# Optimization experiments

Hardware: AMD Instinct MI355X
Metric: run time of the kernel (lower is better)

The kernel has to match this reference:

```python
import jax, jax.numpy as jnp
import numpy as np

GAMMA = 0.999      # EMA momentum
M_PROTO = 10       # prototypes per class
K_CLS = 201        # 200 classes + background
EPS_SK = 0.05      # sinkhorn temperature
SK_ITERS = 3       # sinkhorn iterations
THR = 0.5          # pseudo-gt threshold
D_BB = 768         # backbone dim
D = 512            # projected dim


def _ln(x, g, b, eps=1e-5):
    mu = x.mean(-1, keepdims=True)
    var = ((x - mu) ** 2).mean(-1, keepdims=True)
    return (x - mu) / jnp.sqrt(var + eps) * g + b


def _l2n(x, eps=1e-12):
    n = jnp.linalg.norm(x, axis=-1, keepdims=True)
    return x / jnp.maximum(n, eps)


def _pca_dir(A, niter=10):
    # rank-1 PCA direction (deterministic power iteration; mirrors torch.pca_lowrank(q=1, center=True))
    Ac = A - A.mean(0, keepdims=True)
    v = jnp.ones((A.shape[1],), A.dtype) / jnp.sqrt(jnp.asarray(A.shape[1], A.dtype))
    for _ in range(niter):
        v = Ac.T @ (Ac @ v)
        v = v / jnp.linalg.norm(v)
    u = Ac @ v
    return u / jnp.linalg.norm(u)


def setup_inputs() -> dict:
    key = jax.random.key(0)
    ks = jax.random.split(key, 6)
    B, HW = 16, 1024
    return dict(
        patch_tokens=jax.random.normal(ks[0], (B, HW, D_BB), jnp.float32),
        gt=jax.random.randint(ks[1], (B,), 0, K_CLS - 1),
        proj_w=jax.random.normal(ks[2], (D, D_BB), jnp.float32) * 0.02,
        proj_b=jnp.zeros((D,), jnp.float32),
        feat_g=jnp.ones((D,), jnp.float32),
        feat_b=jnp.zeros((D,), jnp.float32),
        mask_g=jnp.ones((K_CLS,), jnp.float32),
        mask_b=jnp.zeros((K_CLS,), jnp.float32),
        prototypes=jax.random.normal(ks[3], (K_CLS, M_PROTO, D), jnp.float32) * 0.02,
    )


def reference(patch_tokens, gt, proj_w, proj_b, feat_g, feat_b, mask_g, mask_b, prototypes):
    B, HW, _ = patch_tokens.shape
    H = W = int(np.sqrt(HW))
    N = B * HW

    # ----- ged_pseudo_gt (on detached tokens) -----
    U = _pca_dir(patch_tokens.reshape(-1, D_BB))            # [N]
    Us = (U - U.min()) / (U.max() - U.min())
    Us = Us.reshape(B, H, W)
    pseudo_gt = jnp.where(Us < THR, gt[:, None, None], K_CLS - 1)  # [B,H,W]

    # ----- projection + normalization -----
    f = patch_tokens @ proj_w.T + proj_b                    # [B,HW,D]
    _c = _l2n(_ln(f.reshape(N, D), feat_g, feat_b))         # [N,D]
    protos = _l2n(prototypes)                               # buffer is l2-normalized in-place
    masks = jnp.einsum('nd,kmd->nmk', _c, protos)           # [N,M,K] cosine sims
    out_flat = _ln(masks.max(axis=1), mask_g, mask_b)       # [N,K]
    out_seg = out_flat.reshape(B, H, W, K_CLS).transpose(0, 3, 1, 2)  # [B,K,H,W]

    # ----- prototype_learning (vectorized 201-class loop) -----
    gt_seg = pseudo_gt.reshape(-1)                          # [N] int
    pred = jnp.argmax(out_flat, axis=-1)
    correct = (gt_seg == pred).astype(_c.dtype)             # [N]
    proto_logits = _c @ protos.reshape(-1, D).T             # [N, K*M]

    sel = jax.nn.one_hot(gt_seg, K_CLS, dtype=_c.dtype)     # [N,K] class membership
    Bk = sel.sum(0)                                         # pixels per class
    Bk_safe = jnp.where(Bk > 0, Bk, 1.0)

    # masked per-class sinkhorn (all classes in parallel)
    Q = jnp.exp(masks / EPS_SK) * sel[:, None, :]           # [N,M,K]
    sQ = Q.sum((0, 1))                                      # [K]
    Q = Q / jnp.where(sQ > 0, sQ, 1.0)
    for _ in range(SK_ITERS):
        row = Q.sum(0, keepdims=True)                       # [1,M,K] sum over pixels
        Q = Q / jnp.where(row > 0, row, 1.0) / M_PROTO
        col = Q.sum(1, keepdims=True)                       # [N,1,K] sum over prototypes
        Q = Q / jnp.where(col > 0, col, 1.0) / Bk_safe
    Q = Q * Bk                                              # [N,M,K]

    Qn = jnp.take_along_axis(Q, gt_seg[:, None, None], axis=2)[:, :, 0]  # [N,M]
    idx = jnp.argmax(Qn, axis=1)                            # hard assignment per pixel
    proto_target = (idx + M_PROTO * gt_seg).astype(jnp.float32)

    # EMA update: q masked by prediction correctness (m_k applies to both m_q and c_q; m_k^2 = m_k)
    q = jax.nn.one_hot(idx, M_PROTO, dtype=_c.dtype) * correct[:, None]  # [N,M]
    fproto = jnp.einsum('nk,nm,nd->kmd', sel, q, _c)        # per-(class,proto) feature sums
    ncnt = jnp.einsum('nk,nm->km', sel, q)                  # assignment counts
    fnorm = _l2n(fproto)
    upd = (ncnt != 0)[:, :, None]
    new_protos = _l2n(jnp.where(upd, GAMMA * protos + (1.0 - GAMMA) * fnorm, protos))

    return out_seg, proto_logits, proto_target, pseudo_gt, new_protos
```

## Files before the change

### kernel.cpp

```cpp
#include <hip/hip_runtime.h>
#include <cstdint>
#include <cstddef>

typedef _Float16 half8  __attribute__((ext_vector_type(8)));
typedef _Float16 half4v __attribute__((ext_vector_type(4)));
typedef float    f32x4  __attribute__((ext_vector_type(4)));

static constexpr int HWPX = 1024;
static constexpr int NPX  = 16384;
static constexpr int DBB  = 768;
static constexpr int DD   = 512;
static constexpr int KC   = 201;
static constexpr int KM   = 2010;
static constexpr int KMP  = 2048;

static constexpr size_t OFF_XCH    = 0;
static constexpr size_t OFF_TP     = 491520;
static constexpr size_t OFF_COLP   = 492160;
static constexpr size_t OFF_ROW16  = 541312;
static constexpr size_t OFF_ROW3   = 670336;
static constexpr size_t OFF_ROW5   = 678400;
static constexpr size_t OFF_BK     = 686464;
static constexpr size_t OFF_NCNT   = 687488;
static constexpr size_t OFF_FPROTO = 695552;
static constexpr size_t OFF_MAXB   = 4812032;
static constexpr size_t ZTOTAL     = 17984768;
static constexpr size_t OFF_GTSEG  = 17984768;
static constexpr size_t OFF_CORR   = 18050304;
static constexpr size_t OFF_U      = 18115840;
static constexpr size_t OFF_PN     = 18246912;
static constexpr size_t OFF_P16    = 22363392;
static constexpr size_t OFF_C16    = 24460544;
static constexpr size_t OFF_QD     = 41237760;
static constexpr size_t OFF_W16    = 41893120;
static constexpr size_t OFF_MSF    = 42679552;

static constexpr size_t OUT_SEG = 0;
static constexpr size_t OUT_PL  = 3293184;
static constexpr size_t OUT_PT  = 36225024;
static constexpr size_t OUT_PG  = 36241408;
static constexpr size_t OUT_NP  = 36257792;

#define GLDS16(gp, lp) __builtin_amdgcn_global_load_lds( \
    (__attribute__((address_space(1))) const void*)(gp), \
    (__attribute__((address_space(3))) void*)(lp), 16, 0, 0)

static __device__ __forceinline__ float  wredf(float x){
  #pragma unroll
  for (int o=32;o;o>>=1) x += __shfl_down(x,o);
  return x;
}
static __device__ __forceinline__ double wredd(double x){
  #pragma unroll
  for (int o=32;o;o>>=1) x += __shfl_down(x,o);
  return x;
}

template<bool FIRST>
__global__ __launch_bounds__(256) void kPIter2(const float* __restrict__ A,
    const double* __restrict__ Win, const double* __restrict__ Tin, const double* __restrict__ msf,
    double* __restrict__ Wout, double* __restrict__ Tout, double* __restrict__ colout){
  __shared__ double vs[768];
  __shared__ double red[4][12][64];
  __shared__ double sT[4];
  int tid=threadIdx.x, lane=tid&63, w=tid>>6;
  if (FIRST){
    for (int cc=tid; cc<768; cc+=256) vs[cc] = 1.0/sqrt(768.0);
  } else {
    double Ts=0.0;
    #pragma unroll
    for (int p=0;p<8;p++) Ts += Tin[p];
    for (int cc=tid; cc<768; cc+=256){
      double sw=0.0;
      #pragma unroll
      for (int p=0;p<8;p++) sw += Win[p*768+cc];
      vs[cc] = sw - msf[cc]*Ts;
    }
  }
  __syncthreads();
  double vsr[12];
  #pragma unroll
  for (int ch=0;ch<3;ch++)
    #pragma unroll
    for (int e=0;e<4;e++) vsr[ch*4+e] = vs[ch*256 + lane*4 + e];
  int rbase = blockIdx.x*16 + w*4;
  const float* Ab = A + (size_t)rbase*DBB + lane*4;
  double acc[12], cacc[12]; double tloc=0.0;
  #pragma unroll
  for (int j=0;j<12;j++){ acc[j]=0.0; cacc[j]=0.0; }
  #pragma unroll
  for (int i=0;i<4;i++){
    const float* Ar = Ab + (size_t)i*DBB;
    float4 f0 = *(const float4*)(Ar);
    float4 f1 = *(const float4*)(Ar + 256);
    float4 f2 = *(const float4*)(Ar + 512);
    double a[12] = {(double)f0.x,(double)f0.y,(double)f0.z,(double)f0.w,
                    (double)f1.x,(double)f1.y,(double)f1.z,(double)f1.w,
                    (double)f2.x,(double)f2.y,(double)f2.z,(double)f2.w};
    double wp=0.0;
    #pragma unroll
    for (int j=0;j<12;j++) wp += a[j]*vsr[j];
    wp = wredd(wp); wp = __shfl(wp,0);
    #pragma unroll
    for (int j=0;j<12;j++) acc[j] += wp*a[j];
    if (FIRST){
      #pragma unroll
      for (int j=0;j<12;j++) cacc[j] += a[j];
    }
    tloc += wp;
  }
  #pragma unroll
  for (int j=0;j<12;j++) red[w][j][lane]=acc[j];
  if (lane==0) sT[w]=tloc;
  __syncthreads();
  double* dst = Wout + (size_t)(blockIdx.x&7)*768;
  for (int cc=tid; cc<768; cc+=256){
    int chv=cc>>8, rem=cc&255, l=rem>>2, e=rem&3, j=chv*4+e;
    atomicAdd(&dst[cc], red[0][j][l]+red[1][j][l]+red[2][j][l]+red[3][j][l]);
  }
  if (tid==0) atomicAdd(&Tout[blockIdx.x&7], sT[0]+sT[1]+sT[2]+sT[3]);
  if (FIRST){
    __syncthreads();
    #pragma unroll
    for (int j=0;j<12;j++) red[w][j][lane]=cacc[j];
    __syncthreads();
    double* cdst = colout + (size_t)(blockIdx.x&7)*768;
    for (int cc=tid; cc<768; cc+=256){
      int chv=cc>>8, rem=cc&255, l=rem>>2, e=rem&3, j=chv*4+e;
      atomicAdd(&cdst[cc], red[0][j][l]+red[1][j][l]+red[2][j][l]+red[3][j][l]);
    }
  }
}

__global__ __launch_bounds__(256) void kRedM(const double* __restrict__ colp, double* __restrict__ msf){
  for (int cc=threadIdx.x; cc<768; cc+=256){
    double s=0.0;
    #pragma unroll
    for (int p=0;p<8;p++) s += colp[p*768+cc];
    msf[cc] = s * (1.0/16384.0);
  }
}

__global__ __launch_bounds__(256) void kPU2(const float* __restrict__ A, const double* __restrict__ Wp,
    const double* __restrict__ Tp, const double* __restrict__ msf, double* __restrict__ u){
  __shared__ double vs[768];
  __shared__ double sS[4];
  int tid=threadIdx.x, lane=tid&63, w=tid>>6;
  double Ts=0.0;
  #pragma unroll
  for (int p=0;p<8;p++) Ts += Tp[p];
  double sloc=0.0;
  for (int cc=tid; cc<768; cc+=256){
    double sw=0.0;
    #pragma unroll
    for (int p=0;p<8;p++) sw += Wp[p*768+cc];
    double m = msf[cc];
    double v = sw - m*Ts;
    vs[cc] = v;
    sloc += m*v;
  }
  sloc = wredd(sloc);
  if (lane==0) sS[w]=sloc;
  __syncthreads();
  double s = sS[0]+sS[1]+sS[2]+sS[3];
  double vsr[12];
  #pragma unroll
  for (int ch=0;ch<3;ch++)
    #pragma unroll
    for (int e=0;e<4;e++) vsr[ch*4+e] = vs[ch*256 + lane*4 + e];
  int rbase = blockIdx.x*16 + w*4;
  const float* Ab = A + (size_t)rbase*DBB + lane*4;
  #pragma unroll
  for (int i=0;i<4;i++){
    const float* Ar = Ab + (size_t)i*DBB;
    float4 f0 = *(const float4*)(Ar);
    float4 f1 = *(const float4*)(Ar + 256);
    float4 f2 = *(const float4*)(Ar + 512);
    double a[12] = {(double)f0.x,(double)f0.y,(double)f0.z,(double)f0.w,
                    (double)f1.x,(double)f1.y,(double)f1.z,(double)f1.w,
                    (double)f2.x,(double)f2.y,(double)f2.z,(double)f2.w};
    double wp=0.0;
    #pragma unroll
    for (int j=0;j<12;j++) wp += a[j]*vsr[j];
    wp = wredd(wp);
    if (lane==0) u[rbase+i] = wp - s;
  }
}

__global__ __launch_bounds__(1024) void kFin(const double* __restrict__ u, const int* __restrict__ gt,
      float* __restrict__ outPG, int* __restrict__ gtseg, int* __restrict__ Bk){
  __shared__ double smn[16], smx[16];
  __shared__ double sres[2];
  int t = threadIdx.x;
  double mn=1e300, mx=-1e300;
  for (int k=0;k<16;k++){ double x=u[k*1024+t]; mn=fmin(mn,x); mx=fmax(mx,x); }
  #pragma unroll
  for (int o=32;o;o>>=1){ mn=fmin(mn,__shfl_down(mn,o)); mx=fmax(mx,__shfl_down(mx,o)); }
  if ((t&63)==0){ smn[t>>6]=mn; smx[t>>6]=mx; }
  __syncthreads();
  if (t==0){
    for (int i=1;i<16;i++){ mn=fmin(mn,smn[i]); mx=fmax(mx,smx[i]); }
    sres[0]=mn; sres[1]=mx;
  }
  __syncthreads();
  mn=sres[0]; mx=sres[1];
  double inv = 1.0/(mx-mn);
  for (int k=0;k<16;k++){
    int n = k*1024 + t;
    int c0 = gt[k];
    double us = (u[n]-mn)*inv;
    int g = (us < 0.5) ? c0 : 200;
    outPG[n] = (float)g;
    gtseg[n] = g;
    unsigned long long b0 = __ballot(g==c0);
    unsigned long long b1 = __ballot(g==200);
    if ((t&63)==0){
      atomicAdd(&Bk[c0], (int)__popcll(b0));
      atomicAdd(&Bk[200], (int)__popcll(b1));
    }
  }
}

__global__ __launch_bounds__(256) void kPrep(const float* __restrict__ Wp, _Float16* __restrict__ W16,
    const float* __restrict__ PR, float* __restrict__ Pn, _Float16* __restrict__ P16){
  int b = blockIdx.x;
  if (b < 384){
    int i = b*256 + threadIdx.x;
    float4 vv = ((const float4*)Wp)[i];
    half4v h; h[0]=(_Float16)vv.x; h[1]=(_Float16)vv.y; h[2]=(_Float16)vv.z; h[3]=(_Float16)vv.w;
    ((half4v*)W16)[i] = h;
    return;
  }
  int w=threadIdx.x>>6, lane=threadIdx.x&63;
  int km = (b-384)*4 + w;
  if (km >= KM){
    if (km < KMP){
      half8 z;
      #pragma unroll
      for (int i=0;i<8;i++) z[i]=(_Float16)0.0f;
      *(half8*)(P16 + (size_t)km*DD + lane*8) = z;
    }
    return;
  }
  const float* r = PR + (size_t)km*DD + lane*8;
  float4 a = *(const float4*)r, b2 = *(const float4*)(r+4);
  float x[8] = {a.x,a.y,a.z,a.w,b2.x,b2.y,b2.z,b2.w};
  float ss=0;
  #pragma unroll
  for (int i=0;i<8;i++) ss += x[i]*x[i];
  ss = __shfl(wredf(ss),0);
  float nrm = fmaxf(sqrtf(ss), 1e-12f);
  float* pw = Pn + (size_t)km*DD + lane*8;
  half8 h;
  #pragma unroll
  for (int i=0;i<8;i++){ float vv = x[i]/nrm; pw[i]=vv; h[i]=(_Float16)vv; }
  *(half8*)(P16 + (size_t)km*DD + lane*8) = h;
}

__global__ __launch_bounds__(256) void gemm1(const float* __restrict__ Af, const _Float16* __restrict__ Bm,
    _Float16* __restrict__ Ch, const float* __restrict__ bias){
  __shared__ __align__(16) char smem[32768];
  char* As = smem;
  char* Bs = smem + 16384;
  const int tid = threadIdx.x;
  const int lane = tid & 63, w = tid >> 6;
  const int wr = w >> 1, wc = w & 1;
  const int lrow = lane & 15, kg = lane >> 4;
  const int id = blockIdx.x;
  const int xcd = id & 7, pos = id >> 3;
  const int m0 = ((xcd<<4) | (pos>>2)) * 128;
  const int n0 = (pos & 3) * 128;

  f32x4 acc[4][4];
  #pragma unroll
  for (int i=0;i<4;i++)
    #pragma unroll
    for (int j=0;j<4;j++){ f32x4 z = {0.f,0.f,0.f,0.f}; acc[i][j]=z; }

  for (int k0 = 0; k0 < DBB; k0 += 64){
    #pragma unroll
    for (int i=0;i<4;i++){
      int slot = (i*4 + w)*64 + lane;
      int r = slot >> 3, c = slot & 7;
      int cs = c ^ (r & 7);
      GLDS16(Bm + (size_t)(n0+r)*DBB + k0 + cs*8, Bs + (i*4+w)*1024);
    }
    #pragma unroll
    for (int i=0;i<8;i++){
      int slot = i*256 + tid;
      int r = slot >> 4, c4 = slot & 15;
      float4 v = *(const float4*)(Af + (size_t)(m0+r)*DBB + k0 + c4*4);
      half4v h; h[0]=(_Float16)v.x; h[1]=(_Float16)v.y; h[2]=(_Float16)v.z; h[3]=(_Float16)v.w;
      *(half4v*)(As + r*128 + (((c4>>1)^(r&7))<<4) + (c4&1)*8) = h;
    }
    __syncthreads();
    #pragma unroll
    for (int h=0; h<2; h++){
      half8 af[4], bf[4];
      #pragma unroll
      for (int mi=0;mi<4;mi++){
        int ar = wr*64 + mi*16 + lrow;
        af[mi] = *(const half8*)(As + ar*128 + (((h*4+kg) ^ (ar&7))<<4));
      }
      #pragma unroll
      for (int nj=0;nj<4;nj++){
        int br = wc*64 + nj*16 + lrow;
        bf[nj] = *(const half8*)(Bs + br*128 + (((h*4+kg) ^ (br&7))<<4));
      }
      #pragma unroll
      for (int mi=0;mi<4;mi++)
        #pragma unroll
        for (int nj=0;nj<4;nj++)
          acc[mi][nj] = __builtin_amdgcn_mfma_f32_16x16x32_f16(af[mi], bf[nj], acc[mi][nj], 0,0,0);
    }
    __syncthreads();
  }
  _Float16* lsf = (_Float16*)smem;
  #pragma unroll
  for (int h=0; h<2; ++h){
    __syncthreads();
    if (wr == h){
      #pragma unroll
      for (int mi=0;mi<4;mi++){
        int lr = mi*16 + kg*4;
        #pragma unroll
        for (int nj=0;nj<4;nj++){
          int col = wc*64 + nj*16 + lrow;
          float bv = bias[n0 + col];
          #pragma unroll
          for (int r2=0;r2<4;r2++) lsf[(lr+r2)*136 + col] = (_Float16)(acc[mi][nj][r2] + bv);
        }
      }
    }
    __syncthreads();
    #pragma unroll
    for (int it=0; it<4; ++it){
      int idx = it*256 + tid;
      int row = idx >> 4, c8 = idx & 15;
      half8 v = *(const half8*)(lsf + row*136 + c8*8);
      *(half8*)(Ch + (size_t)(m0 + h*64 + row)*DD + n0 + c8*8) = v;
    }
  }
}

__global__ __launch_bounds__(256) void gemm2(const _Float16* __restrict__ Am, const _Float16* __restrict__ Bm,
    float* __restrict__ Cf, unsigned int* __restrict__ maxbuf){
  __shared__ __align__(16) char smem[33792];
  char* As = smem;
  char* Bs = smem + 16384;
  const int tid = threadIdx.x;
  const int lane = tid & 63, w = tid >> 6;
  const int wr = w >> 1, wc = w & 1;
  const int lrow = lane & 15, kg = lane >> 4;
  const int id = blockIdx.x;
  const int xcd = id & 7, pos = id >> 3;
  const int m0 = ((xcd<<4) | (pos>>4)) * 128;
  const int n0 = (pos & 15) * 128;

  f32x4 acc[4][4];
  #pragma unroll
  for (int i=0;i<4;i++)
    #pragma unroll
    for (int j=0;j<4;j++){ f32x4 z = {0.f,0.f,0.f,0.f}; acc[i][j]=z; }

  for (int k0 = 0; k0 < DD; k0 += 64){
    #pragma unroll
    for (int i=0;i<4;i++){
      int slot = (i*4 + w)*64 + lane;
      int r = slot >> 3, c = slot & 7;
      int cs = c ^ (r & 7);
      GLDS16(Am + (size_t)(m0+r)*DD + k0 + cs*8, As + (i*4+w)*1024);
      GLDS16(Bm + (size_t)(n0+r)*DD + k0 + cs*8, Bs + (i*4+w)*1024);
    }
    __syncthreads();
    #pragma unroll
    for (int h=0; h<2; h++){
      half8 af[4], bf[4];
      #pragma unroll
      for (int mi=0;mi<4;mi++){
        int ar = wr*64 + mi*16 + lrow;
        af[mi] = *(const half8*)(As + ar*128 + (((h*4+kg) ^ (ar&7))<<4));
      }
      #pragma unroll
      for (int nj=0;nj<4;nj++){
        int br = wc*64 + nj*16 + lrow;
        bf[nj] = *(const half8*)(Bs + br*128 + (((h*4+kg) ^ (br&7))<<4));
      }
      #pragma unroll
      for (int mi=0;mi<4;mi++)
        #pragma unroll
        for (int nj=0;nj<4;nj++)
          acc[mi][nj] = __builtin_amdgcn_mfma_f32_16x16x32_f16(af[mi], bf[nj], acc[mi][nj], 0,0,0);
    }
    __syncthreads();
  }
  float* lsf = (float*)smem;
  const int cLo = n0/10;
  const int cHi = (n0+127)/10 > 200 ? 200 : (n0+127)/10;
  const int nC = cHi - cLo + 1;
  for (int h=0; h<2; ++h){
    __syncthreads();
    if (wr == h){
      #pragma unroll
      for (int mi=0;mi<4;mi++){
        int lr = mi*16 + kg*4;
        #pragma unroll
        for (int nj=0;nj<4;nj++){
          int col = wc*64 + nj*16 + lrow;
          #pragma unroll
          for (int r2=0;r2<4;r2++) lsf[(lr+r2)*132 + col] = acc[mi][nj][r2];
        }
      }
    }
    __syncthreads();
    #pragma unroll
    for (int it=0; it<8; ++it){
      int idx = it*256 + tid;
      int row = idx >> 5, c4 = idx & 31;
      int gc = n0 + c4*4;
      f32x4 v = *(const f32x4*)(lsf + row*132 + c4*4);
      float* dstp = Cf + (size_t)(m0 + h*64 + row)*KM + gc;
      if (gc + 3 < KM) *(f32x4*)dstp = v;
      else {
        #pragma unroll
        for (int e=0;e<4;e++) if (gc+e < KM) dstp[e] = v[e];
      }
    }
    for (int t = tid; t < 64*nC; t += 256){
      int row = t / nC, c = cLo + t % nC;
      int lo = c*10;     if (lo < n0) lo = n0;
      int hi = c*10+9;   if (hi > n0+127) hi = n0+127;
      float mx = lsf[row*132 + (lo-n0)];
      for (int cc2 = lo+1; cc2 <= hi; ++cc2) mx = fmaxf(mx, lsf[row*132 + (cc2-n0)]);
      atomicMax(&maxbuf[(size_t)(m0 + h*64 + row)*KC + c], __float_as_uint(mx + 4.0f));
    }
  }
}

__global__ __launch_bounds__(256) void kLNl2n(_Float16* __restrict__ C16,
      const float* __restrict__ fg, const float* __restrict__ fb){
  int w=threadIdx.x>>6, lane=threadIdx.x&63;
  int n = blockIdx.x*4 + w;
  _Float16* row = C16 + (size_t)n*DD + lane*8;
  half8 h = *(const half8*)row;
  float x[8];
  #pragma unroll
  for (int i=0;i<8;i++) x[i] = (float)h[i];
  float s=0;
  #pragma unroll
  for (int i=0;i<8;i++) s += x[i];
  float mu = __shfl(wredf(s),0)/512.f;
  float q=0;
  #pragma unroll
  for (int i=0;i<8;i++){ float d=x[i]-mu; q+=d*d; }
  float var = __shfl(wredf(q),0)/512.f;
  float inv = 1.f/sqrtf(var+1e-5f);
  float4 g0 = *(const float4*)(fg+lane*8), g1 = *(const float4*)(fg+lane*8+4);
  float4 b0 = *(const float4*)(fb+lane*8), b1 = *(const float4*)(fb+lane*8+4);
  float gg[8] = {g0.x,g0.y,g0.z,g0.w,g1.x,g1.y,g1.z,g1.w};
  float bb[8] = {b0.x,b0.y,b0.z,b0.w,b1.x,b1.y,b1.z,b1.w};
  float y[8]; float ss=0;
  #pragma unroll
  for (int i=0;i<8;i++){ y[i] = (x[i]-mu)*inv*gg[i]+bb[i]; ss += y[i]*y[i]; }
  float nrm = fmaxf(sqrtf(__shfl(wredf(ss),0)), 1e-12f);
  half8 o;
  #pragma unroll
  for (int i=0;i<8;i++) o[i] = (_Float16)(y[i]/nrm);
  *(half8*)row = o;
}

__global__ __launch_bounds__(256) void kMaxSK(const unsigned int* __restrict__ maxbuf,
    const float* __restrict__ PL, const float* __restrict__ mg,
    const float* __restrict__ mb, const int* __restrict__ gtseg, const int* __restrict__ gt,
    float* __restrict__ outseg, int* __restrict__ corr, float* __restrict__ Qd, float* __restrict__ row16){
  __shared__ float tile[16][205];
  __shared__ float qpart[10][2];
  int tid=threadIdx.x, lane=tid&63, w=tid>>6;
  int n0 = blockIdx.x*16;
  int b = n0>>10, hw0 = n0&1023;
  int c0 = gt[b];
  if (tid<20) qpart[tid>>1][tid&1]=0.f;
  __syncthreads();
  for (int r=0;r<16;r++){
    int n = n0 + r;
    int g = gtseg[n];
    if (tid < KC){
      tile[r][tid] = __uint_as_float(maxbuf[(size_t)n*KC + tid]) - 4.0f;
      if (tid == g){
        const float* src = PL + (size_t)n*KM + g*10;
        int cl = (g==200)?1:0;
        #pragma unroll
        for (int m2=0;m2<5;m2++){
          float2 t2 = *(const float2*)(src + m2*2);
          float e0 = expf(t2.x*20.f), e1 = expf(t2.y*20.f);
          Qd[(size_t)n*10+m2*2]   = e0;
          Qd[(size_t)n*10+m2*2+1] = e1;
          atomicAdd(&qpart[m2*2][cl], e0);
          atomicAdd(&qpart[m2*2+1][cl], e1);
        }
      }
    }
  }
  __syncthreads();
  for (int rr=0; rr<4; ++rr){
    int r = w*4 + rr;
    int n = n0 + r;
    float xv[4]; int ncl=0;
    for (int c=lane;c<KC;c+=64) xv[ncl++] = tile[r][c];
    float ps=0;
    for (int i=0;i<ncl;i++) ps += xv[i];
    float mu = __shfl(wredf(ps),0)*(1.f/201.f);
    float pv=0;
    for (int i=0;i<ncl;i++){ float d=xv[i]-mu; pv+=d*d; }
    float var = __shfl(wredf(pv),0)*(1.f/201.f);
    float inv = 1.f/sqrtf(var+1e-5f);
    float bv=-3.0e38f; int bi=1<<30;
    ncl=0;
    for (int c=lane;c<KC;c+=64){
      float o = (xv[ncl]-mu)*inv*mg[c]+mb[c]; ncl++;
      tile[r][c] = o;
      if (o>bv){ bv=o; bi=c; }
    }
    #pragma unroll
    for (int o2=32;o2;o2>>=1){
      float ov=__shfl_down(bv,o2); int oi=__shfl_down(bi,o2);
      if (ov>bv||(ov==bv&&oi<bi)){bv=ov;bi=oi;}
    }
    if (lane==0) corr[n] = (bi==gtseg[n])?1:0;
  }
  __syncthreads();
  if (tid<20){
    int m=tid>>1, cl=tid&1;
    atomicAdd(&row16[(size_t)(blockIdx.x&15)*2016 + m*KC + (cl?200:c0)], qpart[m][cl]);
  }
  for (int idx=tid; idx<KC*4; idx+=256){
    int c = idx>>2, j4 = idx&3;
    float4 v;
    v.x = tile[j4*4+0][c];
    v.y = tile[j4*4+1][c];
    v.z = tile[j4*4+2][c];
    v.w = tile[j4*4+3][c];
    *(float4*)(outseg + (((size_t)b*KC+c)<<10) + hw0 + j4*4) = v;
  }
}

__global__ __launch_bounds__(256) void kSKpass(float* __restrict__ Qd, const int* __restrict__ gtseg,
      const int* __restrict__ gt, const float* __restrict__ rin, int rin_parts,
      float* __restrict__ rout, const int* __restrict__ Bk){
  __shared__ float rin2[10][2];
  __shared__ double part[4][10][2];
  int n = blockIdx.x*256+threadIdx.x;
  int c0 = gt[blockIdx.x>>2];
  if (threadIdx.x < 20){
    int m = threadIdx.x>>1, cl = threadIdx.x&1;
    int cls = cl?200:c0;
    float s=0;
    for (int p=0;p<rin_parts;p++) s += rin[(size_t)p*2016 + m*KC + cls];
    rin2[m][cl]=s;
  }
  __syncthreads();
  int g = gtseg[n];
  int cl = (g==200)?1:0;
  double q[10]; double col=0.0;
  #pragma unroll
  for (int m=0;m<10;m++){
    double r = (double)rin2[m][cl];
    double t = (double)Qd[(size_t)n*10+m];
    if (r>0.0) t = t/r;
    t = t/10.0;
    q[m]=t; col+=t;
  }
  double cs = (col>0.0)? col : 1.0;
  int bk = Bk[g];
  double bs = (bk>0)? (double)bk : 1.0;
  double inv = 1.0/(cs*bs);
  int w=threadIdx.x>>6, lane=threadIdx.x&63;
  #pragma unroll
  for (int m=0;m<10;m++){
    double t = q[m]*inv;
    Qd[(size_t)n*10+m] = (float)t;
    double p0 = (g==c0)? t:0.0;
    double p1 = (g==200)? t:0.0;
    p0=wredd(p0); p1=wredd(p1);
    if (lane==0){ part[w][m][0]=p0; part[w][m][1]=p1; }
  }
  __syncthreads();
  if (threadIdx.x < 20){
    int m = threadIdx.x>>1, cl2 = threadIdx.x&1;
    double t = part[0][m][cl2]+part[1][m][cl2]+part[2][m][cl2]+part[3][m][cl2];
    atomicAdd(&rout[m*KC + (cl2?200:c0)], (float)t);
  }
}

__global__ __launch_bounds__(256) void kSKEMA(const float* __restrict__ Qd, const int* __restrict__ gtseg,
      const float* __restrict__ r5, const int* __restrict__ corr, const _Float16* __restrict__ C16,
      float* __restrict__ outPT, float* __restrict__ fproto, int* __restrict__ ncnt){
  int w=threadIdx.x>>6, lane=threadIdx.x&63;
  int n = blockIdx.x*4+w;
  int g = gtseg[n];
  float tv = -1.0f;
  if (lane<10){
    float r = r5[lane*KC+g];
    float t = Qd[(size_t)n*10+lane];
    if (r>0.f) t = t/r;
    tv = t*0.1f;
  }
  float bv = tv; int bi = lane;
  #pragma unroll
  for (int o=8;o;o>>=1){
    float ov = __shfl_down(bv,o); int oi = __shfl_down(bi,o);
    if (ov>bv || (ov==bv && oi<bi)){ bv=ov; bi=oi; }
  }
  bi = __shfl(bi, 0);
  if (lane==0) outPT[n] = (float)(bi + 10*g);
  if (corr[n]){
    half8 hc = *(const half8*)(C16 + (size_t)n*DD + lane*8);
    float* dst = fproto + ((size_t)g*10+bi)*DD + lane*8;
    #pragma unroll
    for (int i=0;i<8;i++) atomicAdd(dst+i, (float)hc[i]);
    if (lane==0) atomicAdd(&ncnt[g*10+bi], 1);
  }
}

__global__ __launch_bounds__(256) void kEMAfin(const float* __restrict__ fproto, const int* __restrict__ ncnt,
     const float* __restrict__ Pn, float* __restrict__ outNP){
  int w=threadIdx.x>>6, lane=threadIdx.x&63;
  int km = blockIdx.x*4+w;
  if (km>=KM) return;
  const float* fr = fproto + (size_t)km*DD + lane*8;
  float fp[8]; float ss=0;
  #pragma unroll
  for (int i=0;i<8;i++){ fp[i]=fr[i]; ss+=fp[i]*fp[i]; }
  float n1 = fmaxf(sqrtf(__shfl(wredf(ss),0)), 1e-12f);
  int cnt = ncnt[km];
  const float* pr = Pn + (size_t)km*DD + lane*8;
  float t[8]; float s2=0;
  #pragma unroll
  for (int i=0;i<8;i++){
    float pv = pr[i];
    float tv = cnt ? (0.999f*pv + 0.001f*(fp[i]/n1)) : pv;
    t[i]=tv; s2+=tv*tv;
  }
  float n2 = fmaxf(sqrtf(__shfl(wredf(s2),0)), 1e-12f);
  float* dst = outNP + (size_t)km*DD + lane*8;
  #pragma unroll
  for (int i=0;i<8;i++) dst[i] = t[i]/n2;
}

extern "C" void kernel_launch(void* const* d_in, const int* in_sizes, int n_in,
                              void* d_out, int out_size, void* d_ws, size_t ws_size,
                              hipStream_t stream) {
  const float* A   = (const float*)d_in[0];
  const int*   gt  = (const int*)d_in[1];
  const float* Wp  = (const float*)d_in[2];
  const float* pb  = (const float*)d_in[3];
  const float* fg  = (const float*)d_in[4];
  const float* fb  = (const float*)d_in[5];
  const float* mg  = (const float*)d_in[6];
  const float* mb  = (const float*)d_in[7];
  const float* PR  = (const float*)d_in[8];
  float* out = (float*)d_out;
  char* ws = (char*)d_ws;

  double* xch    = (double*)(ws+OFF_XCH);
  double* Tp     = (double*)(ws+OFF_TP);
  double* colp   = (double*)(ws+OFF_COLP);
  float*  row16  = (float*)(ws+OFF_ROW16);
  float*  row3   = (float*)(ws+OFF_ROW3);
  float*  row5   = (float*)(ws+OFF_ROW5);
  int*    Bk     = (int*)(ws+OFF_BK);
  int*    ncnt   = (int*)(ws+OFF_NCNT);
  float*  fproto = (float*)(ws+OFF_FPROTO);
  unsigned int* maxbuf = (unsigned int*)(ws+OFF_MAXB);
  int*    gtseg  = (int*)(ws+OFF_GTSEG);
  int*    corr   = (int*)(ws+OFF_CORR);
  double* u      = (double*)(ws+OFF_U);
  float*  Pn     = (float*)(ws+OFF_PN);
  _Float16* P16  = (_Float16*)(ws+OFF_P16);
  _Float16* C16  = (_Float16*)(ws+OFF_C16);
  float*  Qd     = (float*)(ws+OFF_QD);
  _Float16* W16  = (_Float16*)(ws+OFF_W16);
  double* msf    = (double*)(ws+OFF_MSF);

  hipMemsetAsync(ws, 0, ZTOTAL, stream);

  kPIter2<true><<<1024,256,0,stream>>>(A, nullptr, nullptr, nullptr, xch, Tp, colp);
  kRedM<<<1,256,0,stream>>>(colp, msf);
  for (int t=1;t<10;t++){
    kPIter2<false><<<1024,256,0,stream>>>(A, xch+(size_t)(t-1)*8*768, Tp+(t-1)*8, msf,
                                          xch+(size_t)t*8*768, Tp+t*8, nullptr);
  }
  kPU2<<<1024,256,0,stream>>>(A, xch+(size_t)9*8*768, Tp+9*8, msf, u);
  kFin<<<1,1024,0,stream>>>(u, gt, out+OUT_PG, gtseg, Bk);

  kPrep<<<896,256,0,stream>>>(Wp, W16, PR, Pn, P16);

  gemm1<<<512,256,0,stream>>>(A, W16, C16, pb);
  kLNl2n<<<4096,256,0,stream>>>(C16, fg, fb);

  gemm2<<<2048,256,0,stream>>>(C16, P16, out+OUT_PL, maxbuf);

  kMaxSK<<<1024,256,0,stream>>>(maxbuf, out+OUT_PL, mg, mb, gtseg, gt, out+OUT_SEG, corr, Qd, row16);

  kSKpass<<<64,256,0,stream>>>(Qd, gtseg, gt, row16, 16, row3, Bk);
  kSKpass<<<64,256,0,stream>>>(Qd, gtseg, gt, row3, 1, row5, Bk);
  kSKEMA<<<4096,256,0,stream>>>(Qd, gtseg, row5, corr, C16, out+OUT_PT, fproto, ncnt);

  kEMAfin<<<503,256,0,stream>>>(fproto, ncnt, Pn, out+OUT_NP);
}
```

Measured before the change: 415.3 us.

## Enlarge gemm2 tiles to 256x256 with double-buffered LDS prefetch

Rewrites the prototype-logit GEMM to use 256x256 output tiles per 512-thread block, double-buffered LDS staging so the next K slice loads while MFMAs run, and s_setprio around the compute loop. The larger tile halves the redundant A/B global loads per output. The epilogue is reworked for the wider tile, writing in four 64-row phases. In exchange it uses 128KB of LDS and 128 accumulator registers per thread, which limits occupancy. The grid shrinks from 2048 to 512 blocks.

```diff
diff --git a/kernel.cpp b/kernel.cpp
--- a/kernel.cpp
+++ b/kernel.cpp
@@ -343,96 +343,109 @@
   }
 }
 
-__global__ __launch_bounds__(256) void gemm2(const _Float16* __restrict__ Am, const _Float16* __restrict__ Bm,
+__global__ __launch_bounds__(512, 2) void gemm2(const _Float16* __restrict__ Am, const _Float16* __restrict__ Bm,
     float* __restrict__ Cf, unsigned int* __restrict__ maxbuf){
-  __shared__ __align__(16) char smem[33792];
-  char* As = smem;
-  char* Bs = smem + 16384;
+  __shared__ __align__(16) char lds[131072];
   const int tid = threadIdx.x;
-  const int lane = tid & 63, w = tid >> 6;
-  const int wr = w >> 1, wc = w & 1;
+  const int lane = tid & 63, wid = tid >> 6;
+  const int wr = wid >> 2, wc = wid & 3;
   const int lrow = lane & 15, kg = lane >> 4;
   const int id = blockIdx.x;
-  const int xcd = id & 7, pos = id >> 3;
-  const int m0 = ((xcd<<4) | (pos>>4)) * 128;
-  const int n0 = (pos & 15) * 128;
-
-  f32x4 acc[4][4];
-  #pragma unroll
-  for (int i=0;i<4;i++)
+  const int nt = id & 7, mt = id >> 3;
+  const int m0 = mt * 256, n0 = nt * 256;
+
+  f32x4 acc[8][4];
+  #pragma unroll
+  for (int i=0;i<8;i++)
     #pragma unroll
     for (int j=0;j<4;j++){ f32x4 z = {0.f,0.f,0.f,0.f}; acc[i][j]=z; }
 
-  for (int k0 = 0; k0 < DD; k0 += 64){
-    #pragma unroll
-    for (int i=0;i<4;i++){
-      int slot = (i*4 + w)*64 + lane;
-      int r = slot >> 3, c = slot & 7;
-      int cs = c ^ (r & 7);
-      GLDS16(Am + (size_t)(m0+r)*DD + k0 + cs*8, As + (i*4+w)*1024);
-      GLDS16(Bm + (size_t)(n0+r)*DD + k0 + cs*8, Bs + (i*4+w)*1024);
-    }
-    __syncthreads();
-    #pragma unroll
-    for (int h=0; h<2; h++){
-      half8 af[4], bf[4];
-      #pragma unroll
-      for (int mi=0;mi<4;mi++){
-        int ar = wr*64 + mi*16 + lrow;
-        af[mi] = *(const half8*)(As + ar*128 + (((h*4+kg) ^ (ar&7))<<4));
-      }
+  #define STAGE2(kt, buf) { \
+    int k0 = (kt)*64; \
+    char* dA = lds + (buf)*65536; \
+    char* dB = dA + 32768; \
+    _Pragma("unroll") \
+    for (int i=0;i<4;i++){ \
+      int slot = i*512 + tid; \
+      int r = slot >> 3, c = slot & 7; \
+      int cs = c ^ (r & 7); \
+      GLDS16(Am + (size_t)(m0+r)*DD + k0 + cs*8, dA + slot*16); \
+      GLDS16(Bm + (size_t)(n0+r)*DD + k0 + cs*8, dB + slot*16); \
+    } }
+
+  STAGE2(0, 0);
+  __syncthreads();
+  for (int kt = 0; kt < 8; ++kt){
+    if (kt < 7) STAGE2(kt+1, (kt+1)&1);
+    const char* sA = lds + (kt&1)*65536;
+    const char* sB = sA + 32768;
+    __builtin_amdgcn_s_setprio(1);
+    #pragma unroll
+    for (int ks=0; ks<2; ks++){
+      half8 bf[4];
       #pragma unroll
       for (int nj=0;nj<4;nj++){
         int br = wc*64 + nj*16 + lrow;
-        bf[nj] = *(const half8*)(Bs + br*128 + (((h*4+kg) ^ (br&7))<<4));
+        bf[nj] = *(const half8*)(sB + br*128 + (((ks*4+kg) ^ (br&7))<<4));
       }
       #pragma unroll
-      for (int mi=0;mi<4;mi++)
+      for (int mi=0;mi<8;mi++){
+        int ar = wr*128 + mi*16 + lrow;
+        half8 af = *(const half8*)(sA + ar*128 + (((ks*4+kg) ^ (ar&7))<<4));
         #pragma unroll
         for (int nj=0;nj<4;nj++)
-          acc[mi][nj] = __builtin_amdgcn_mfma_f32_16x16x32_f16(af[mi], bf[nj], acc[mi][nj], 0,0,0);
-    }
-    __syncthreads();
-  }
-  float* lsf = (float*)smem;
+          acc[mi][nj] = __builtin_amdgcn_mfma_f32_16x16x32_f16(af, bf[nj], acc[mi][nj], 0,0,0);
+      }
+    }
+    __builtin_amdgcn_s_setprio(0);
+    __syncthreads();
+  }
+  #undef STAGE2
+
+  float* lsf = (float*)lds;
   const int cLo = n0/10;
-  const int cHi = (n0+127)/10 > 200 ? 200 : (n0+127)/10;
-  const int nC = cHi - cLo + 1;
-  for (int h=0; h<2; ++h){
-    __syncthreads();
-    if (wr == h){
-      #pragma unroll
-      for (int mi=0;mi<4;mi++){
-        int lr = mi*16 + kg*4;
+  int cHiA = (n0+255)/10; if (cHiA > 200) cHiA = 200;
+  const int nC = cHiA - cLo + 1;
+  for (int e=0; e<4; ++e){
+    __syncthreads();
+    if (wr == (e>>1)){
+      int mbase = (e&1)*4;
+      #pragma unroll
+      for (int mq=0; mq<4; mq++){
+        int lr = mq*16 + kg*4;
         #pragma unroll
         for (int nj=0;nj<4;nj++){
           int col = wc*64 + nj*16 + lrow;
           #pragma unroll
-          for (int r2=0;r2<4;r2++) lsf[(lr+r2)*132 + col] = acc[mi][nj][r2];
+          for (int r2=0;r2<4;r2++)
+            lsf[(lr+r2)*260 + col] = acc[mbase+mq][nj][r2];
         }
       }
     }
     __syncthreads();
+    int grow0 = m0 + e*64;
     #pragma unroll
     for (int it=0; it<8; ++it){
-      int idx = it*256 + tid;
-      int row = idx >> 5, c4 = idx & 31;
+      int idx = it*512 + tid;
+      int row = idx >> 6, c4 = idx & 63;
       int gc = n0 + c4*4;
-      f32x4 v = *(const f32x4*)(lsf + row*132 + c4*4);
-      float* dstp = Cf + (size_t)(m0 + h*64 + row)*KM + gc;
-      if (gc + 3 < KM) *(f32x4*)dstp = v;
-      else {
-        #pragma unroll
-        for (int e=0;e<4;e++) if (gc+e < KM) dstp[e] = v[e];
+      if (gc < KM){
+        f32x4 v = *(const f32x4*)(lsf + row*260 + c4*4);
+        float* dstp = Cf + (size_t)(grow0+row)*KM + gc;
+        if (gc + 3 < KM) *(f32x4*)dstp = v;
+        else {
+          #pragma unroll
+          for (int e2=0;e2<4;e2++) if (gc+e2 < KM) dstp[e2] = v[e2];
+        }
       }
     }
-    for (int t = tid; t < 64*nC; t += 256){
+    for (int t = tid; t < 64*nC; t += 512){
       int row = t / nC, c = cLo + t % nC;
       int lo = c*10;     if (lo < n0) lo = n0;
-      int hi = c*10+9;   if (hi > n0+127) hi = n0+127;
-      float mx = lsf[row*132 + (lo-n0)];
-      for (int cc2 = lo+1; cc2 <= hi; ++cc2) mx = fmaxf(mx, lsf[row*132 + (cc2-n0)]);
-      atomicMax(&maxbuf[(size_t)(m0 + h*64 + row)*KC + c], __float_as_uint(mx + 4.0f));
+      int hi = c*10+9;   if (hi > n0+255) hi = n0+255;
+      float mx = lsf[row*260 + (lo-n0)];
+      for (int cc2 = lo+1; cc2 <= hi; ++cc2) mx = fmaxf(mx, lsf[row*260 + (cc2-n0)]);
+      atomicMax(&maxbuf[(size_t)(grow0+row)*KC + c], __float_as_uint(mx + 4.0f));
     }
   }
 }
@@ -698,7 +711,7 @@
   gemm1<<<512,256,0,stream>>>(A, W16, C16, pb);
   kLNl2n<<<4096,256,0,stream>>>(C16, fg, fb);
 
-  gemm2<<<2048,256,0,stream>>>(C16, P16, out+OUT_PL, maxbuf);
+  gemm2<<<512,512,0,stream>>>(C16, P16, out+OUT_PL, maxbuf);
 
   kMaxSK<<<1024,256,0,stream>>>(maxbuf, out+OUT_PL, mg, mb, gtseg, gt, out+OUT_SEG, corr, Qd, row16);
 
```

Result: no change. 408.8 us (-1.6%).
